# Performance work log

Hardware: AMD Instinct MI355X
Metric: run time of the kernel (lower is better)

## Reference

```python
import jax, jax.numpy as jnp
import numpy as np

N = 100000
E = 1600000
EVENT_DIM = 64
HID = 128


def setup_inputs() -> dict:
    key = jax.random.key(0)
    ks = jax.random.split(key, 12)
    def lin(kw, kb, fan_in, fan_out):
        bound = 1.0 / np.sqrt(fan_in)
        W = jax.random.uniform(kw, (fan_in, fan_out), jnp.float32, -bound, bound)
        b = jax.random.uniform(kb, (fan_out,), jnp.float32, -bound, bound)
        return W, b
    base_feat = jax.random.normal(ks[0], (N, HID), jnp.float32)
    event_vector = jax.random.normal(ks[1], (N, EVENT_DIM), jnp.float32)
    edge_index = jax.random.randint(ks[2], (2, E), 0, N, jnp.int64)
    W_proj, b_proj = lin(ks[3], ks[4], EVENT_DIM, HID)
    W_gcn, b_gcn = lin(ks[5], ks[6], HID, HID)
    W_gate, b_gate = lin(ks[7], ks[8], 2 * HID, HID)
    W_fuse, b_fuse = lin(ks[9], ks[10], 2 * HID, HID)
    return {"base_feat": base_feat, "event_vector": event_vector,
            "edge_index": edge_index,
            "W_proj": W_proj, "b_proj": b_proj,
            "W_gcn": W_gcn, "b_gcn": b_gcn,
            "W_gate": W_gate, "b_gate": b_gate,
            "W_fuse": W_fuse, "b_fuse": b_fuse}


def gcn_conv(x, edge_index, W, b, n):
    # PyG GCNConv: x @ W, add self-loops, symmetric deg^-1/2 normalization,
    # scatter-sum into target nodes, then + bias.
    x = x @ W  # [N, H]
    loop = jnp.arange(n, dtype=edge_index.dtype)
    src = jnp.concatenate([edge_index[0], loop])
    dst = jnp.concatenate([edge_index[1], loop])
    deg = jax.ops.segment_sum(jnp.ones_like(dst, dtype=x.dtype), dst, num_segments=n)
    dis = jnp.where(deg > 0, jax.lax.rsqrt(deg), 0.0)
    norm = dis[src] * dis[dst]  # [E+N]
    msgs = x[src] * norm[:, None]  # gather + scale
    out = jax.ops.segment_sum(msgs, dst, num_segments=n)  # scatter-sum
    return out + b


def reference(base_feat, event_vector, edge_index,
              W_proj, b_proj, W_gcn, b_gcn, W_gate, b_gate, W_fuse, b_fuse):
    n = base_feat.shape[0]
    event_feat = jax.nn.relu(event_vector @ W_proj + b_proj)
    diffused = jax.nn.relu(gcn_conv(event_feat, edge_index, W_gcn, b_gcn, n))
    gate_in = jnp.concatenate([base_feat, diffused], axis=-1)
    gate = jax.nn.sigmoid(gate_in @ W_gate + b_gate)
    corrected = base_feat * (1.0 - gate) + diffused * gate
    fuse_in = jnp.concatenate([base_feat, corrected], axis=-1)
    return jax.nn.relu(fuse_in @ W_fuse + b_fuse)
```

## Files before the change

### kernel.cpp

```cpp
#include <hip/hip_runtime.h>


typedef unsigned short inj_u16;
typedef unsigned int   inj_u32;
typedef __attribute__((ext_vector_type(8))) short bf16x8;
typedef __attribute__((ext_vector_type(4))) float f32x4;

static constexpr int INJ_N  = 100000;
static constexpr int INJ_E  = 1600000;
static constexpr int INJ_H  = 128;
static constexpr int INJ_D  = 64;
static constexpr int INJ_NB = 196;
static constexpr int INJ_CH = 6400;
static constexpr int INJ_PB = 250;

__device__ __forceinline__ float inj_b2f(inj_u16 h){
  union { inj_u32 u; float f; } c; c.u = ((inj_u32)h) << 16; return c.f;
}
__device__ __forceinline__ inj_u16 inj_f2b(float x){
  union { inj_u32 u; float f; } c; c.f = x;
  return (inj_u16)((c.u + 0x7FFFu + ((c.u >> 16) & 1u)) >> 16);
}
__device__ __forceinline__ float inj_lo(inj_u32 w){ return inj_b2f((inj_u16)(w & 0xFFFFu)); }
__device__ __forceinline__ float inj_hi(inj_u32 w){ return inj_b2f((inj_u16)(w >> 16)); }
__device__ __forceinline__ inj_u32 inj_pack(float a, float b){
  return ((inj_u32)inj_f2b(b) << 16) | (inj_u32)inj_f2b(a);
}
__device__ __forceinline__ float inj_ld1(const void* p, size_t i, int f32){
  return f32 ? ((const float*)p)[i] : inj_b2f(((const inj_u16*)p)[i]);
}
__device__ __forceinline__ float2 inj_ld2(const void* p, size_t pair, int f32){
  if (f32) return ((const float2*)p)[pair];
  inj_u32 w = ((const inj_u32*)p)[pair];
  float2 r; r.x = inj_lo(w); r.y = inj_hi(w);
  return r;
}

__global__ void inj_flags(const int* eidx, const inj_u32* base, int* flags){
  int l = threadIdx.x & 63;
  unsigned long long nz = __ballot(eidx[2*l + 1] != 0);
  inj_u32 ex = (base[l] >> 7) & 0xFFu;
  unsigned long long inr = __ballot(ex >= 100u && ex <= 135u);
  if (threadIdx.x == 0){
    flags[0] = (nz == 0ull) ? 1 : 0;
    flags[1] = (__popcll(inr) >= 56) ? 0 : 1;
  }
}

__device__ __forceinline__ int inj_eread(const int* e, size_t i, int w64){
  return w64 ? e[2*i] : e[i];
}

__global__ __launch_bounds__(256) void inj_bhist(const int* eidx, int* bhp,
                                                 const int* flags){
  __shared__ int h[INJ_NB];
  const int tid = threadIdx.x;
  const int e0 = blockIdx.x * INJ_CH;
  const int w64 = flags[0];
  for (int b = tid; b < INJ_NB; b += 256) h[b] = 0;
  __syncthreads();
  for (int i = tid; i < INJ_CH; i += 256){
    int dst = inj_eread(eidx, (size_t)INJ_E + e0 + i, w64);
    atomicAdd(&h[dst >> 9], 1);
  }
  __syncthreads();
  for (int b = tid; b < INJ_NB; b += 256)
    if (h[b]) atomicAdd(&bhp[b*16], h[b]);
}

__global__ void inj_bscan(const int* bhp, int* bbase, int* bcurA, int* rowp){
  __shared__ int s[256];
  int tid = threadIdx.x;
  int v = (tid < INJ_NB) ? bhp[tid*16] : 0;
  s[tid] = v; __syncthreads();
  for (int off = 1; off < 256; off <<= 1){
    int t = (tid >= off) ? s[tid - off] : 0;
    __syncthreads();
    s[tid] += t;
    __syncthreads();
  }
  if (tid < INJ_NB){
    int base = s[tid] - v;
    bbase[tid]    = base;
    bcurA[tid*16] = base;
  }
  if (tid == 0){ bbase[INJ_NB] = INJ_E; rowp[INJ_N] = INJ_E; }
}

__global__ __launch_bounds__(256) void inj_passA(
    const int* eidx, int* bcurA, inj_u32* pairs, const int* flags){
  __shared__ inj_u32 sedge[INJ_CH];
  __shared__ unsigned char sbkt[INJ_CH];
  __shared__ int scnt[INJ_NB];
  __shared__ int scur[INJ_NB];
  const int tid = threadIdx.x;
  const int e0 = blockIdx.x * INJ_CH;
  const int w64 = flags[0];
  for (int b = tid; b < INJ_NB; b += 256) scnt[b] = 0;
  __syncthreads();
  for (int i = tid; i < INJ_CH; i += 256){
    int src = inj_eread(eidx, (size_t)(e0 + i), w64);
    int dst = inj_eread(eidx, (size_t)INJ_E + e0 + i, w64);
    int b = dst >> 9;
    sedge[i] = (inj_u32)src | ((inj_u32)(dst & 511) << 17);
    sbkt[i] = (unsigned char)b;
    atomicAdd(&scnt[b], 1);
  }
  __syncthreads();
  for (int b = tid; b < INJ_NB; b += 256){
    int c = scnt[b];
    scur[b] = c ? atomicAdd(&bcurA[b*16], c) : 0;
  }
  __syncthreads();
  for (int i = tid; i < INJ_CH; i += 256){
    int b = sbkt[i];
    int pos = atomicAdd(&scur[b], 1);
    pairs[pos] = sedge[i];
  }
}

__global__ __launch_bounds__(256) void inj_passB(
    const inj_u32* pairs, const int* bbase, int* rowp, float* dis, int* es){
  __shared__ int lcnt[512];
  __shared__ int lcur[512];
  __shared__ int ls[512];
  __shared__ int ws[256];
  const int b = blockIdx.x, tid = threadIdx.x;
  const int beg = bbase[b], endp = bbase[b+1];
  const int nbase = b << 9;
  const int nn = min(512, INJ_N - nbase);
  for (int i = tid; i < 512; i += 256) lcnt[i] = 0;
  __syncthreads();
  for (int p = beg + tid; p < endp; p += 256)
    atomicAdd(&lcnt[pairs[p] >> 17], 1);
  __syncthreads();
  int v0 = lcnt[2*tid], v1 = lcnt[2*tid + 1];
  int psum = v0 + v1;
  ws[tid] = psum; __syncthreads();
  for (int off = 1; off < 256; off <<= 1){
    int t = (tid >= off) ? ws[tid - off] : 0;
    __syncthreads();
    ws[tid] += t;
    __syncthreads();
  }
  int ex0 = ws[tid] - psum;
  ls[2*tid]     = ex0;
  ls[2*tid + 1] = ex0 + v0;
  __syncthreads();
  for (int i = tid; i < nn; i += 256){
    int ex = beg + ls[i];
    rowp[nbase + i] = ex;
    lcur[i] = ex;
    dis[nbase + i] = rsqrtf((float)(lcnt[i] + 1));
  }
  __syncthreads();
  for (int p = beg + tid; p < endp; p += 256){
    inj_u32 w = pairs[p];
    int pos = atomicAdd(&lcur[w >> 17], 1);
    es[pos] = (int)(w & 0x1FFFFu);
  }
}

__global__ void inj_wfrag(const void* Wgate, const void* Wfuse,
                          const void* Wp, const void* Wg,
                          inj_u16* wfrag, inj_u16* wpf, inj_u16* wgf2,
                          const int* flags){
  int t = blockIdx.x*256 + threadIdx.x;
  int f32 = flags[1];
  const void* W; inj_u16* dst; int kbase, n;
  if (t < 8192){
    int mat = t >> 12, r = t & 4095;
    int ct = r >> 9, kk = (r >> 6) & 7, lane = r & 63;
    W = mat ? Wfuse : Wgate;
    dst = wfrag + (size_t)mat*32768 + ((ct*8 + kk)*64 + lane)*8;
    kbase = kk*32 + (lane>>4)*8;
    n = ct*16 + (lane & 15);
  } else if (t < 9216){
    int r = t - 8192;
    int ct = r >> 7, kk = (r >> 6) & 1, lane = r & 63;
    W = Wp;
    dst = wpf + ((ct*2 + kk)*64 + lane)*8;
    kbase = kk*32 + (lane>>4)*8;
    n = ct*16 + (lane & 15);
  } else {
    int r = t - 9216;
    int ct = r >> 8, kk = (r >> 6) & 3, lane = r & 63;
    W = Wg;
    dst = wgf2 + ((ct*4 + kk)*64 + lane)*8;
    kbase = kk*32 + (lane>>4)*8;
    n = ct*16 + (lane & 15);
  }
  #pragma unroll
  for (int j=0;j<8;j++)
    dst[j] = inj_f2b(inj_ld1(W, (size_t)(kbase + j)*INJ_H + n, f32));
}

__global__ __launch_bounds__(256) void inj_projgcn(
    const void* ev, const void* bp,
    const inj_u16* wpf, const inj_u16* wgf2,
    const float* dis, inj_u32* x, const int* flags){
  __shared__ __align__(16) inj_u16 s_a [ 8*136];
  __shared__ __align__(16) inj_u16 s_ef[16*136];
  __shared__ float s_dis[16];
  const int f32 = flags[1];
  const int tid = threadIdx.x;
  const int n0 = blockIdx.x * 16;

  if (tid < 128){
    int m = tid >> 3, g = tid & 7;
    uint4 v;
    if (!f32){
      v = ((const uint4*)ev)[(size_t)(n0 + m)*8 + g];
    } else {
      const float4* e4 = (const float4*)ev;
      float4 x0 = e4[(size_t)(n0 + m)*16 + g*2];
      float4 x1 = e4[(size_t)(n0 + m)*16 + g*2 + 1];
      v.x = inj_pack(x0.x, x0.y); v.y = inj_pack(x0.z, x0.w);
      v.z = inj_pack(x1.x, x1.y); v.w = inj_pack(x1.z, x1.w);
    }
    *(uint4*)(s_a + g*136 + m*8) = v;
  }
  if (tid < 16) s_dis[tid] = dis[n0 + tid];
  __syncthreads();

  const int lane = tid & 63, wave = tid >> 6;
  const int mrow = lane & 15, quad = lane >> 4;

  float bp0 = inj_ld1(bp, (wave*2    )*16 + mrow, f32);
  float bp1 = inj_ld1(bp, (wave*2 + 1)*16 + mrow, f32);
  f32x4 acc[2] = {{bp0,bp0,bp0,bp0},{bp1,bp1,bp1,bp1}};
  #pragma unroll
  for (int kk = 0; kk < 2; kk++){
    bf16x8 a  = *(const bf16x8*)(s_a + (kk*4 + quad)*136 + mrow*8);
    bf16x8 b0 = *(const bf16x8*)(wpf + (((wave*2    )*2 + kk)*64 + lane)*8);
    bf16x8 b1 = *(const bf16x8*)(wpf + (((wave*2 + 1)*2 + kk)*64 + lane)*8);
    acc[0] = __builtin_amdgcn_mfma_f32_16x16x32_bf16(a, b0, acc[0], 0, 0, 0);
    acc[1] = __builtin_amdgcn_mfma_f32_16x16x32_bf16(a, b1, acc[1], 0, 0, 0);
  }
  #pragma unroll
  for (int t = 0; t < 2; t++){
    int col = (wave*2 + t)*16 + mrow;
    int goff = (col >> 3)*136 + (col & 7);
    #pragma unroll
    for (int r = 0; r < 4; r++){
      int row = quad*4 + r;
      s_ef[goff + row*8] = inj_f2b(fmaxf(acc[t][r], 0.f));
    }
  }
  __syncthreads();

  f32x4 acc2[2] = {{0.f,0.f,0.f,0.f},{0.f,0.f,0.f,0.f}};
  #pragma unroll
  for (int kk = 0; kk < 4; kk++){
    bf16x8 a  = *(const bf16x8*)(s_ef + (kk*4 + quad)*136 + mrow*8);
    bf16x8 b0 = *(const bf16x8*)(wgf2 + (((wave*2    )*4 + kk)*64 + lane)*8);
    bf16x8 b1 = *(const bf16x8*)(wgf2 + (((wave*2 + 1)*4 + kk)*64 + lane)*8);
    acc2[0] = __builtin_amdgcn_mfma_f32_16x16x32_bf16(a, b0, acc2[0], 0, 0, 0);
    acc2[1] = __builtin_amdgcn_mfma_f32_16x16x32_bf16(a, b1, acc2[1], 0, 0, 0);
  }
  inj_u16* xo = (inj_u16*)x;
  #pragma unroll
  for (int t = 0; t < 2; t++){
    int col = (wave*2 + t)*16 + mrow;
    #pragma unroll
    for (int r = 0; r < 4; r++){
      int row = quad*4 + r;
      xo[(size_t)(n0 + row)*INJ_H + col] = inj_f2b(acc2[t][r] * s_dis[row]);
    }
  }
}

__global__ void inj_gather(const inj_u32* x, const int* row_ptr, const int* es,
                           const float* dis, const void* b_gcn,
                           inj_u32* dif, const int* flags){
  const int tid = threadIdx.x;
  const int lane = tid & 63, wv = tid >> 6;
  const int n = blockIdx.x*4 + wv;
  const float dd = dis[n];
  inj_u32 xv = x[(size_t)n*64 + lane];
  float a0 = inj_lo(xv), a1 = inj_hi(xv);
  const int beg = row_ptr[n], end = row_ptr[n+1];
  for (int c = beg; c < end; c += 64){
    int m = end - c; if (m > 64) m = 64;
    int srcv = (lane < m) ? es[c + lane] : 0;
    int j = 0;
    for (; j + 8 <= m; j += 8){
      int s0 = __shfl(srcv, j  ), s1 = __shfl(srcv, j+1);
      int s2 = __shfl(srcv, j+2), s3 = __shfl(srcv, j+3);
      int s4 = __shfl(srcv, j+4), s5 = __shfl(srcv, j+5);
      int s6 = __shfl(srcv, j+6), s7 = __shfl(srcv, j+7);
      inj_u32 v0 = x[(size_t)s0*64 + lane];
      inj_u32 v1 = x[(size_t)s1*64 + lane];
      inj_u32 v2 = x[(size_t)s2*64 + lane];
      inj_u32 v3 = x[(size_t)s3*64 + lane];
      inj_u32 v4 = x[(size_t)s4*64 + lane];
      inj_u32 v5 = x[(size_t)s5*64 + lane];
      inj_u32 v6 = x[(size_t)s6*64 + lane];
      inj_u32 v7 = x[(size_t)s7*64 + lane];
      a0 += inj_lo(v0) + inj_lo(v1) + inj_lo(v2) + inj_lo(v3)
          + inj_lo(v4) + inj_lo(v5) + inj_lo(v6) + inj_lo(v7);
      a1 += inj_hi(v0) + inj_hi(v1) + inj_hi(v2) + inj_hi(v3)
          + inj_hi(v4) + inj_hi(v5) + inj_hi(v6) + inj_hi(v7);
    }
    for (; j + 4 <= m; j += 4){
      int s0 = __shfl(srcv, j  ), s1 = __shfl(srcv, j+1);
      int s2 = __shfl(srcv, j+2), s3 = __shfl(srcv, j+3);
      inj_u32 v0 = x[(size_t)s0*64 + lane];
      inj_u32 v1 = x[(size_t)s1*64 + lane];
      inj_u32 v2 = x[(size_t)s2*64 + lane];
      inj_u32 v3 = x[(size_t)s3*64 + lane];
      a0 += inj_lo(v0) + inj_lo(v1) + inj_lo(v2) + inj_lo(v3);
      a1 += inj_hi(v0) + inj_hi(v1) + inj_hi(v2) + inj_hi(v3);
    }
    for (; j < m; ++j){
      inj_u32 v = x[(size_t)__shfl(srcv, j)*64 + lane];
      a0 += inj_lo(v);
      a1 += inj_hi(v);
    }
  }
  float2 bg = inj_ld2(b_gcn, lane, flags[1]);
  dif[(size_t)n*64 + lane] = inj_pack(fmaxf(fmaf(a0, dd, bg.x), 0.f),
                                      fmaxf(fmaf(a1, dd, bg.y), 0.f));
}

__global__ __launch_bounds__(256) void InjectionLayer_91130616086689_kernel(
    const void* base, const void* bgate, const void* bfuse,
    const inj_u16* wgf, const inj_u16* wff,
    const inj_u32* dif, void* outp, const int* flags){
  __shared__ __align__(16) inj_u16 s_b[16*136];
  __shared__ __align__(16) inj_u16 s_d[16*136];
  __shared__ __align__(16) inj_u16 s_c[16*136];
  const int f32 = flags[1];
  const int tid = threadIdx.x;
  const int n0 = blockIdx.x * 16;

  {
    int m = tid >> 4, g = tid & 15;
    uint4 vb;
    if (!f32){
      vb = ((const uint4*)base)[(size_t)(n0 + m)*16 + g];
    } else {
      const float4* b4 = (const float4*)base;
      float4 x0 = b4[(size_t)(n0 + m)*32 + g*2];
      float4 x1 = b4[(size_t)(n0 + m)*32 + g*2 + 1];
      vb.x = inj_pack(x0.x, x0.y); vb.y = inj_pack(x0.z, x0.w);
      vb.z = inj_pack(x1.x, x1.y); vb.w = inj_pack(x1.z, x1.w);
    }
    *(uint4*)(s_b + g*136 + m*8) = vb;
    uint4 vd = ((const uint4*)dif)[(size_t)(n0 + m)*16 + g];
    *(uint4*)(s_d + g*136 + m*8) = vd;
  }
  __syncthreads();

  const int lane = tid & 63, wave = tid >> 6;
  const int mrow = lane & 15, quad = lane >> 4;

  f32x4 accg[2] = {{0.f,0.f,0.f,0.f},{0.f,0.f,0.f,0.f}};
  #pragma unroll
  for (int kk = 0; kk < 8; kk++){
    const inj_u16* mat = (kk < 4) ? s_b : s_d;
    int g = (kk & 3)*4 + quad;
    bf16x8 a = *(const bf16x8*)(mat + g*136 + mrow*8);
    bf16x8 b0 = *(const bf16x8*)(wgf + (((wave*2    )*8 + kk)*64 + lane)*8);
    bf16x8 b1 = *(const bf16x8*)(wgf + (((wave*2 + 1)*8 + kk)*64 + lane)*8);
    accg[0] = __builtin_amdgcn_mfma_f32_16x16x32_bf16(a, b0, accg[0], 0, 0, 0);
    accg[1] = __builtin_amdgcn_mfma_f32_16x16x32_bf16(a, b1, accg[1], 0, 0, 0);
  }

  #pragma unroll
  for (int t = 0; t < 2; t++){
    int col = (wave*2 + t)*16 + mrow;
    float bg = inj_ld1(bgate, col, f32);
    int gk = (col >> 5)*4 + ((col >> 3) & 3), jj = col & 7;
    #pragma unroll
    for (int r = 0; r < 4; r++){
      int row = quad*4 + r;
      float gate = 1.f/(1.f + expf(-(accg[t][r] + bg)));
      int off = gk*136 + row*8 + jj;
      float bb = inj_b2f(s_b[off]);
      float dd = inj_b2f(s_d[off]);
      s_c[off] = inj_f2b(bb*(1.f - gate) + dd*gate);
    }
  }
  __syncthreads();

  f32x4 accf[2] = {{0.f,0.f,0.f,0.f},{0.f,0.f,0.f,0.f}};
  #pragma unroll
  for (int kk = 0; kk < 8; kk++){
    const inj_u16* mat = (kk < 4) ? s_b : s_c;
    int g = (kk & 3)*4 + quad;
    bf16x8 a = *(const bf16x8*)(mat + g*136 + mrow*8);
    bf16x8 b0 = *(const bf16x8*)(wff + (((wave*2    )*8 + kk)*64 + lane)*8);
    bf16x8 b1 = *(const bf16x8*)(wff + (((wave*2 + 1)*8 + kk)*64 + lane)*8);
    accf[0] = __builtin_amdgcn_mfma_f32_16x16x32_bf16(a, b0, accf[0], 0, 0, 0);
    accf[1] = __builtin_amdgcn_mfma_f32_16x16x32_bf16(a, b1, accf[1], 0, 0, 0);
  }
  #pragma unroll
  for (int t = 0; t < 2; t++){
    int col = (wave*2 + t)*16 + mrow;
    float bf = inj_ld1(bfuse, col, f32);
    #pragma unroll
    for (int r = 0; r < 4; r++){
      int row = quad*4 + r;
      float v = fmaxf(accf[t][r] + bf, 0.f);
      size_t oi = (size_t)(n0 + row)*INJ_H + col;
      if (f32) ((float*)outp)[oi] = v;
      else     ((inj_u16*)outp)[oi] = inj_f2b(v);
    }
  }
}

extern "C" __attribute__((visibility("default")))
void kernel_launch(void* const* d_in, const int* in_sizes, int n_in,
                   void* d_out, int out_size, void* d_ws, size_t ws_size,
                   hipStream_t stream) {
  const void* base  = d_in[0];
  const void* ev    = d_in[1];
  const int*  eidx  = (const int*)d_in[2];
  const void* Wp    = d_in[3];
  const void* bp    = d_in[4];
  const void* Wg    = d_in[5];
  const void* bg    = d_in[6];
  const void* Wgate = d_in[7];
  const void* bgate = d_in[8];
  const void* Wfuse = d_in[9];
  const void* bfuse = d_in[10];

  inj_u32* x = (inj_u32*)d_out;

  char* ws = (char*)d_ws;
  inj_u32* dif    = (inj_u32*)(ws);
  int*     es     = (int*)    (ws + 25600000);
  int*     bhp    = (int*)    (ws + 32000000);
  int*     bbase  = (int*)    (ws + 32065536);
  int*     rowp   = (int*)    (ws + 32400000);
  int*     bcurA  = (int*)    (ws + 32800016);
  float*   dis    = (float*)  (ws + 33200016);
  int*     flags  = (int*)    (ws + 33601600);
  inj_u16* wfrag  = (inj_u16*)(ws + 33601664);
  inj_u32* pairs  = (inj_u32*)(ws);
  inj_u16* wpf    = (inj_u16*)(ws + 25550848);
  inj_u16* wgf2   = (inj_u16*)(ws + 25567232);

  hipMemsetAsync(bhp, 0, (size_t)INJ_NB*64, stream);
  inj_flags  <<<1, 64, 0, stream>>>(eidx, (const inj_u32*)base, flags);
  inj_bhist  <<<INJ_PB, 256, 0, stream>>>(eidx, bhp, flags);
  inj_wfrag  <<<44, 256, 0, stream>>>(Wgate, Wfuse, Wp, Wg, wfrag, wpf, wgf2, flags);
  inj_bscan  <<<1, 256, 0, stream>>>(bhp, bbase, bcurA, rowp);
  inj_passA  <<<INJ_PB, 256, 0, stream>>>(eidx, bcurA, pairs, flags);
  inj_passB  <<<INJ_NB, 256, 0, stream>>>(pairs, bbase, rowp, dis, es);
  inj_projgcn<<<INJ_N/16, 256, 0, stream>>>(ev, bp, wpf, wgf2, dis, x, flags);
  inj_gather <<<INJ_N/4, 256, 0, stream>>>(x, rowp, es, dis, bg, dif, flags);
  InjectionLayer_91130616086689_kernel<<<INJ_N/16, 256, 0, stream>>>(
      base, bgate, bfuse, wfrag, wfrag + 32768, dif, d_out, flags);
}
```

Measured before the change: 318.0 us.

## Fuse GCN neighbor gather into gate/fuse MLP kernel via shared memory

Removes the separate gather kernel and performs the CSR neighbor aggregation inside the final gate/fuse kernel. Each wave aggregates 4 nodes and writes the diffused bf16 rows straight into shared memory, so the diffused intermediate is never written to or reread from global memory. x moves from the output buffer into workspace, and the weight-fragment buffers are relocated to avoid overlap. The cost is fewer waves per node (4 nodes per wave, sequential) and possible load imbalance or reduced memory-level parallelism in the gather stage.

```diff
diff --git a/kernel.cpp b/kernel.cpp
--- a/kernel.cpp
+++ b/kernel.cpp
@@ -270,69 +270,18 @@
   }
 }
 
-__global__ void inj_gather(const inj_u32* x, const int* row_ptr, const int* es,
-                           const float* dis, const void* b_gcn,
-                           inj_u32* dif, const int* flags){
-  const int tid = threadIdx.x;
-  const int lane = tid & 63, wv = tid >> 6;
-  const int n = blockIdx.x*4 + wv;
-  const float dd = dis[n];
-  inj_u32 xv = x[(size_t)n*64 + lane];
-  float a0 = inj_lo(xv), a1 = inj_hi(xv);
-  const int beg = row_ptr[n], end = row_ptr[n+1];
-  for (int c = beg; c < end; c += 64){
-    int m = end - c; if (m > 64) m = 64;
-    int srcv = (lane < m) ? es[c + lane] : 0;
-    int j = 0;
-    for (; j + 8 <= m; j += 8){
-      int s0 = __shfl(srcv, j  ), s1 = __shfl(srcv, j+1);
-      int s2 = __shfl(srcv, j+2), s3 = __shfl(srcv, j+3);
-      int s4 = __shfl(srcv, j+4), s5 = __shfl(srcv, j+5);
-      int s6 = __shfl(srcv, j+6), s7 = __shfl(srcv, j+7);
-      inj_u32 v0 = x[(size_t)s0*64 + lane];
-      inj_u32 v1 = x[(size_t)s1*64 + lane];
-      inj_u32 v2 = x[(size_t)s2*64 + lane];
-      inj_u32 v3 = x[(size_t)s3*64 + lane];
-      inj_u32 v4 = x[(size_t)s4*64 + lane];
-      inj_u32 v5 = x[(size_t)s5*64 + lane];
-      inj_u32 v6 = x[(size_t)s6*64 + lane];
-      inj_u32 v7 = x[(size_t)s7*64 + lane];
-      a0 += inj_lo(v0) + inj_lo(v1) + inj_lo(v2) + inj_lo(v3)
-          + inj_lo(v4) + inj_lo(v5) + inj_lo(v6) + inj_lo(v7);
-      a1 += inj_hi(v0) + inj_hi(v1) + inj_hi(v2) + inj_hi(v3)
-          + inj_hi(v4) + inj_hi(v5) + inj_hi(v6) + inj_hi(v7);
-    }
-    for (; j + 4 <= m; j += 4){
-      int s0 = __shfl(srcv, j  ), s1 = __shfl(srcv, j+1);
-      int s2 = __shfl(srcv, j+2), s3 = __shfl(srcv, j+3);
-      inj_u32 v0 = x[(size_t)s0*64 + lane];
-      inj_u32 v1 = x[(size_t)s1*64 + lane];
-      inj_u32 v2 = x[(size_t)s2*64 + lane];
-      inj_u32 v3 = x[(size_t)s3*64 + lane];
-      a0 += inj_lo(v0) + inj_lo(v1) + inj_lo(v2) + inj_lo(v3);
-      a1 += inj_hi(v0) + inj_hi(v1) + inj_hi(v2) + inj_hi(v3);
-    }
-    for (; j < m; ++j){
-      inj_u32 v = x[(size_t)__shfl(srcv, j)*64 + lane];
-      a0 += inj_lo(v);
-      a1 += inj_hi(v);
-    }
-  }
-  float2 bg = inj_ld2(b_gcn, lane, flags[1]);
-  dif[(size_t)n*64 + lane] = inj_pack(fmaxf(fmaf(a0, dd, bg.x), 0.f),
-                                      fmaxf(fmaf(a1, dd, bg.y), 0.f));
-}
-
 __global__ __launch_bounds__(256) void InjectionLayer_91130616086689_kernel(
     const void* base, const void* bgate, const void* bfuse,
     const inj_u16* wgf, const inj_u16* wff,
-    const inj_u32* dif, void* outp, const int* flags){
+    const inj_u32* x, const int* rowp, const int* es, const float* dis,
+    const void* bgcn, void* outp, const int* flags){
   __shared__ __align__(16) inj_u16 s_b[16*136];
   __shared__ __align__(16) inj_u16 s_d[16*136];
   __shared__ __align__(16) inj_u16 s_c[16*136];
   const int f32 = flags[1];
   const int tid = threadIdx.x;
   const int n0 = blockIdx.x * 16;
+  const int lane = tid & 63, wave = tid >> 6;
 
   {
     int m = tid >> 4, g = tid & 15;
@@ -347,12 +296,63 @@
       vb.z = inj_pack(x1.x, x1.y); vb.w = inj_pack(x1.z, x1.w);
     }
     *(uint4*)(s_b + g*136 + m*8) = vb;
-    uint4 vd = ((const uint4*)dif)[(size_t)(n0 + m)*16 + g];
-    *(uint4*)(s_d + g*136 + m*8) = vd;
-  }
-  __syncthreads();
-
-  const int lane = tid & 63, wave = tid >> 6;
+  }
+
+  {
+    float2 bg = inj_ld2(bgcn, lane, f32);
+    const int doff = (lane >> 2)*136 + ((2*lane) & 7);
+    for (int t = 0; t < 4; t++){
+      const int m = wave*4 + t;
+      const int n = n0 + m;
+      const float dd = dis[n];
+      inj_u32 xv = x[(size_t)n*64 + lane];
+      float a0 = inj_lo(xv), a1 = inj_hi(xv);
+      const int beg = rowp[n], end = rowp[n+1];
+      for (int c = beg; c < end; c += 64){
+        int mm = end - c; if (mm > 64) mm = 64;
+        int srcv = (lane < mm) ? es[c + lane] : 0;
+        int j = 0;
+        for (; j + 8 <= mm; j += 8){
+          int s0 = __shfl(srcv, j  ), s1 = __shfl(srcv, j+1);
+          int s2 = __shfl(srcv, j+2), s3 = __shfl(srcv, j+3);
+          int s4 = __shfl(srcv, j+4), s5 = __shfl(srcv, j+5);
+          int s6 = __shfl(srcv, j+6), s7 = __shfl(srcv, j+7);
+          inj_u32 v0 = x[(size_t)s0*64 + lane];
+          inj_u32 v1 = x[(size_t)s1*64 + lane];
+          inj_u32 v2 = x[(size_t)s2*64 + lane];
+          inj_u32 v3 = x[(size_t)s3*64 + lane];
+          inj_u32 v4 = x[(size_t)s4*64 + lane];
+          inj_u32 v5 = x[(size_t)s5*64 + lane];
+          inj_u32 v6 = x[(size_t)s6*64 + lane];
+          inj_u32 v7 = x[(size_t)s7*64 + lane];
+          a0 += inj_lo(v0) + inj_lo(v1) + inj_lo(v2) + inj_lo(v3)
+              + inj_lo(v4) + inj_lo(v5) + inj_lo(v6) + inj_lo(v7);
+          a1 += inj_hi(v0) + inj_hi(v1) + inj_hi(v2) + inj_hi(v3)
+              + inj_hi(v4) + inj_hi(v5) + inj_hi(v6) + inj_hi(v7);
+        }
+        for (; j + 4 <= mm; j += 4){
+          int s0 = __shfl(srcv, j  ), s1 = __shfl(srcv, j+1);
+          int s2 = __shfl(srcv, j+2), s3 = __shfl(srcv, j+3);
+          inj_u32 v0 = x[(size_t)s0*64 + lane];
+          inj_u32 v1 = x[(size_t)s1*64 + lane];
+          inj_u32 v2 = x[(size_t)s2*64 + lane];
+          inj_u32 v3 = x[(size_t)s3*64 + lane];
+          a0 += inj_lo(v0) + inj_lo(v1) + inj_lo(v2) + inj_lo(v3);
+          a1 += inj_hi(v0) + inj_hi(v1) + inj_hi(v2) + inj_hi(v3);
+        }
+        for (; j < mm; ++j){
+          inj_u32 v = x[(size_t)__shfl(srcv, j)*64 + lane];
+          a0 += inj_lo(v);
+          a1 += inj_hi(v);
+        }
+      }
+      a0 = fmaxf(fmaf(a0, dd, bg.x), 0.f);
+      a1 = fmaxf(fmaf(a1, dd, bg.y), 0.f);
+      *(inj_u32*)(s_d + doff + m*8) = inj_pack(a0, a1);
+    }
+  }
+  __syncthreads();
+
   const int mrow = lane & 15, quad = lane >> 4;
 
   f32x4 accg[2] = {{0.f,0.f,0.f,0.f},{0.f,0.f,0.f,0.f}};
@@ -426,21 +426,19 @@
   const void* Wfuse = d_in[9];
   const void* bfuse = d_in[10];
 
-  inj_u32* x = (inj_u32*)d_out;
-
   char* ws = (char*)d_ws;
-  inj_u32* dif    = (inj_u32*)(ws);
+  inj_u32* x      = (inj_u32*)(ws);
+  inj_u32* pairs  = (inj_u32*)(ws);
   int*     es     = (int*)    (ws + 25600000);
   int*     bhp    = (int*)    (ws + 32000000);
+  inj_u16* wpf    = (inj_u16*)(ws + 32016384);
+  inj_u16* wgf2   = (inj_u16*)(ws + 32032768);
   int*     bbase  = (int*)    (ws + 32065536);
   int*     rowp   = (int*)    (ws + 32400000);
   int*     bcurA  = (int*)    (ws + 32800016);
   float*   dis    = (float*)  (ws + 33200016);
   int*     flags  = (int*)    (ws + 33601600);
   inj_u16* wfrag  = (inj_u16*)(ws + 33601664);
-  inj_u32* pairs  = (inj_u32*)(ws);
-  inj_u16* wpf    = (inj_u16*)(ws + 25550848);
-  inj_u16* wgf2   = (inj_u16*)(ws + 25567232);
 
   hipMemsetAsync(bhp, 0, (size_t)INJ_NB*64, stream);
   inj_flags  <<<1, 64, 0, stream>>>(eidx, (const inj_u32*)base, flags);
@@ -450,7 +448,7 @@
   inj_passA  <<<INJ_PB, 256, 0, stream>>>(eidx, bcurA, pairs, flags);
   inj_passB  <<<INJ_NB, 256, 0, stream>>>(pairs, bbase, rowp, dis, es);
   inj_projgcn<<<INJ_N/16, 256, 0, stream>>>(ev, bp, wpf, wgf2, dis, x, flags);
-  inj_gather <<<INJ_N/4, 256, 0, stream>>>(x, rowp, es, dis, bg, dif, flags);
   InjectionLayer_91130616086689_kernel<<<INJ_N/16, 256, 0, stream>>>(
-      base, bgate, bfuse, wfrag, wfrag + 32768, dif, d_out, flags);
-}
+      base, bgate, bfuse, wfrag, wfrag + 32768,
+      x, rowp, es, dis, bg, d_out, flags);
+}
```

Result: faster. 309.1 us, median of 2 (-2.8%).

## Slice x into 16-column panels so gather working set fits cache

Applied to the files above, without the earlier changes.

The projected GCN features are now stored as eight column slices of 16 bf16 values per node instead of row-major 128-wide rows. The gather kernel becomes persistent (2048 blocks), and each block handles one slice, so concurrently running blocks touch a 3.2MB slice that can stay resident in L2/MALL. Each wave processes 8 edges in parallel, with 8 lanes covering the slice's columns, and reduces across groups with shuffles. Edge indices are loaded non-temporally and output is stored non-temporally. The cost is that edge lists are reread once per slice, there is extra shuffle reduction, and weight-fragment workspace offsets move to avoid overlap.

```diff
diff --git a/kernel.cpp b/kernel.cpp
--- a/kernel.cpp
+++ b/kernel.cpp
@@ -198,7 +198,7 @@
 __global__ __launch_bounds__(256) void inj_projgcn(
     const void* ev, const void* bp,
     const inj_u16* wpf, const inj_u16* wgf2,
-    const float* dis, inj_u32* x, const int* flags){
+    const float* dis, inj_u32* x2, const int* flags){
   __shared__ __align__(16) inj_u16 s_a [ 8*136];
   __shared__ __align__(16) inj_u16 s_ef[16*136];
   __shared__ float s_dis[16];
@@ -258,69 +258,68 @@
     acc2[0] = __builtin_amdgcn_mfma_f32_16x16x32_bf16(a, b0, acc2[0], 0, 0, 0);
     acc2[1] = __builtin_amdgcn_mfma_f32_16x16x32_bf16(a, b1, acc2[1], 0, 0, 0);
   }
-  inj_u16* xo = (inj_u16*)x;
+  inj_u16* xo = (inj_u16*)x2;
   #pragma unroll
   for (int t = 0; t < 2; t++){
     int col = (wave*2 + t)*16 + mrow;
+    int slice = col >> 4;
     #pragma unroll
     for (int r = 0; r < 4; r++){
       int row = quad*4 + r;
-      xo[(size_t)(n0 + row)*INJ_H + col] = inj_f2b(acc2[t][r] * s_dis[row]);
-    }
-  }
-}
-
-__global__ void inj_gather(const inj_u32* x, const int* row_ptr, const int* es,
-                           const float* dis, const void* b_gcn,
-                           inj_u32* dif, const int* flags){
+      xo[((size_t)slice*INJ_N + (n0 + row))*16 + (col & 15)] =
+          inj_f2b(acc2[t][r] * s_dis[row]);
+    }
+  }
+}
+
+__global__ __launch_bounds__(256, 8) void inj_gather(
+    const inj_u32* x2, const int* rowp, const int* es,
+    const float* dis, const void* bgcn, inj_u32* dif, const int* flags){
   const int tid = threadIdx.x;
   const int lane = tid & 63, wv = tid >> 6;
-  const int n = blockIdx.x*4 + wv;
-  const float dd = dis[n];
-  inj_u32 xv = x[(size_t)n*64 + lane];
-  float a0 = inj_lo(xv), a1 = inj_hi(xv);
-  const int beg = row_ptr[n], end = row_ptr[n+1];
-  for (int c = beg; c < end; c += 64){
-    int m = end - c; if (m > 64) m = 64;
-    int srcv = (lane < m) ? es[c + lane] : 0;
-    int j = 0;
-    for (; j + 8 <= m; j += 8){
-      int s0 = __shfl(srcv, j  ), s1 = __shfl(srcv, j+1);
-      int s2 = __shfl(srcv, j+2), s3 = __shfl(srcv, j+3);
-      int s4 = __shfl(srcv, j+4), s5 = __shfl(srcv, j+5);
-      int s6 = __shfl(srcv, j+6), s7 = __shfl(srcv, j+7);
-      inj_u32 v0 = x[(size_t)s0*64 + lane];
-      inj_u32 v1 = x[(size_t)s1*64 + lane];
-      inj_u32 v2 = x[(size_t)s2*64 + lane];
-      inj_u32 v3 = x[(size_t)s3*64 + lane];
-      inj_u32 v4 = x[(size_t)s4*64 + lane];
-      inj_u32 v5 = x[(size_t)s5*64 + lane];
-      inj_u32 v6 = x[(size_t)s6*64 + lane];
-      inj_u32 v7 = x[(size_t)s7*64 + lane];
-      a0 += inj_lo(v0) + inj_lo(v1) + inj_lo(v2) + inj_lo(v3)
-          + inj_lo(v4) + inj_lo(v5) + inj_lo(v6) + inj_lo(v7);
-      a1 += inj_hi(v0) + inj_hi(v1) + inj_hi(v2) + inj_hi(v3)
-          + inj_hi(v4) + inj_hi(v5) + inj_hi(v6) + inj_hi(v7);
-    }
-    for (; j + 4 <= m; j += 4){
-      int s0 = __shfl(srcv, j  ), s1 = __shfl(srcv, j+1);
-      int s2 = __shfl(srcv, j+2), s3 = __shfl(srcv, j+3);
-      inj_u32 v0 = x[(size_t)s0*64 + lane];
-      inj_u32 v1 = x[(size_t)s1*64 + lane];
-      inj_u32 v2 = x[(size_t)s2*64 + lane];
-      inj_u32 v3 = x[(size_t)s3*64 + lane];
-      a0 += inj_lo(v0) + inj_lo(v1) + inj_lo(v2) + inj_lo(v3);
-      a1 += inj_hi(v0) + inj_hi(v1) + inj_hi(v2) + inj_hi(v3);
-    }
-    for (; j < m; ++j){
-      inj_u32 v = x[(size_t)__shfl(srcv, j)*64 + lane];
-      a0 += inj_lo(v);
-      a1 += inj_hi(v);
-    }
-  }
-  float2 bg = inj_ld2(b_gcn, lane, flags[1]);
-  dif[(size_t)n*64 + lane] = inj_pack(fmaxf(fmaf(a0, dd, bg.x), 0.f),
-                                      fmaxf(fmaf(a1, dd, bg.y), 0.f));
+  const int s = blockIdx.x & 7;
+  const int g = lane >> 3, c = lane & 7;
+  const inj_u32* xs = x2 + (size_t)s * INJ_N * 8;
+  float2 bg = inj_ld2(bgcn, (size_t)(s*8 + c), flags[1]);
+  const int wbase = (blockIdx.x >> 3)*4 + wv;
+  const int wstr  = (int)(gridDim.x >> 3)*4;
+  for (int n = wbase; n < INJ_N; n += wstr){
+    const float dd = dis[n];
+    inj_u32 xv = xs[(size_t)n*8 + c];
+    float a0 = 0.f, a1 = 0.f;
+    const int beg = rowp[n], end = rowp[n+1];
+    int k = beg;
+    for (; k + 16 <= end; k += 16){
+      int s0 = __builtin_nontemporal_load(es + k + g);
+      int s1 = __builtin_nontemporal_load(es + k + 8 + g);
+      inj_u32 v0 = xs[(size_t)s0*8 + c];
+      inj_u32 v1 = xs[(size_t)s1*8 + c];
+      a0 += inj_lo(v0) + inj_lo(v1);
+      a1 += inj_hi(v0) + inj_hi(v1);
+    }
+    for (; k + 8 <= end; k += 8){
+      int s0 = __builtin_nontemporal_load(es + k + g);
+      inj_u32 v0 = xs[(size_t)s0*8 + c];
+      a0 += inj_lo(v0);
+      a1 += inj_hi(v0);
+    }
+    if (k < end && g < end - k){
+      int s0 = __builtin_nontemporal_load(es + k + g);
+      inj_u32 v0 = xs[(size_t)s0*8 + c];
+      a0 += inj_lo(v0);
+      a1 += inj_hi(v0);
+    }
+    a0 += __shfl_xor(a0, 8);  a1 += __shfl_xor(a1, 8);
+    a0 += __shfl_xor(a0, 16); a1 += __shfl_xor(a1, 16);
+    a0 += __shfl_xor(a0, 32); a1 += __shfl_xor(a1, 32);
+    if (g == 0){
+      a0 += inj_lo(xv);
+      a1 += inj_hi(xv);
+      float r0 = fmaxf(fmaf(a0, dd, bg.x), 0.f);
+      float r1 = fmaxf(fmaf(a1, dd, bg.y), 0.f);
+      __builtin_nontemporal_store(inj_pack(r0, r1), dif + (size_t)n*64 + s*8 + c);
+    }
+  }
 }
 
 __global__ __launch_bounds__(256) void InjectionLayer_91130616086689_kernel(
@@ -426,21 +425,21 @@
   const void* Wfuse = d_in[9];
   const void* bfuse = d_in[10];
 
-  inj_u32* x = (inj_u32*)d_out;
+  inj_u32* x2 = (inj_u32*)d_out;
 
   char* ws = (char*)d_ws;
   inj_u32* dif    = (inj_u32*)(ws);
+  inj_u32* pairs  = (inj_u32*)(ws);
   int*     es     = (int*)    (ws + 25600000);
   int*     bhp    = (int*)    (ws + 32000000);
+  inj_u16* wpf    = (inj_u16*)(ws + 32016384);
+  inj_u16* wgf2   = (inj_u16*)(ws + 32032768);
   int*     bbase  = (int*)    (ws + 32065536);
   int*     rowp   = (int*)    (ws + 32400000);
   int*     bcurA  = (int*)    (ws + 32800016);
   float*   dis    = (float*)  (ws + 33200016);
   int*     flags  = (int*)    (ws + 33601600);
   inj_u16* wfrag  = (inj_u16*)(ws + 33601664);
-  inj_u32* pairs  = (inj_u32*)(ws);
-  inj_u16* wpf    = (inj_u16*)(ws + 25550848);
-  inj_u16* wgf2   = (inj_u16*)(ws + 25567232);
 
   hipMemsetAsync(bhp, 0, (size_t)INJ_NB*64, stream);
   inj_flags  <<<1, 64, 0, stream>>>(eidx, (const inj_u32*)base, flags);
@@ -449,8 +448,8 @@
   inj_bscan  <<<1, 256, 0, stream>>>(bhp, bbase, bcurA, rowp);
   inj_passA  <<<INJ_PB, 256, 0, stream>>>(eidx, bcurA, pairs, flags);
   inj_passB  <<<INJ_NB, 256, 0, stream>>>(pairs, bbase, rowp, dis, es);
-  inj_projgcn<<<INJ_N/16, 256, 0, stream>>>(ev, bp, wpf, wgf2, dis, x, flags);
-  inj_gather <<<INJ_N/4, 256, 0, stream>>>(x, rowp, es, dis, bg, dif, flags);
+  inj_projgcn<<<INJ_N/16, 256, 0, stream>>>(ev, bp, wpf, wgf2, dis, x2, flags);
+  inj_gather <<<2048, 256, 0, stream>>>(x2, rowp, es, dis, bg, dif, flags);
   InjectionLayer_91130616086689_kernel<<<INJ_N/16, 256, 0, stream>>>(
       base, bgate, bfuse, wfrag, wfrag + 32768, dif, d_out, flags);
 }
```

Measured after the change: 472.6 us. 48.6% more time.
